# Optimization experiments

Measured on AMD Instinct MI355X. Metric: run time of the kernel, lower is better.

The kernel has to match this reference:

```python
import jax, jax.numpy as jnp
import numpy as np

N_NODES = 100000
N_EDGES = 1600000
F_IN, F_HID, F_OUT = 256, 128, 32


def setup_inputs() -> dict:
    key = jax.random.key(0)
    k1, k2, k3, k4 = jax.random.split(key, 4)
    x = jax.random.normal(k1, (N_NODES, F_IN), dtype=jnp.float32)
    edge_index = jax.random.randint(k2, (2, N_EDGES), 0, N_NODES, dtype=jnp.int64)
    W1 = jax.random.normal(k3, (F_IN, F_HID), dtype=jnp.float32) * (1.0 / np.sqrt(F_IN))
    b1 = jnp.zeros((F_HID,), dtype=jnp.float32)
    W2 = jax.random.normal(k4, (F_HID, F_OUT), dtype=jnp.float32) * (1.0 / np.sqrt(F_HID))
    b2 = jnp.zeros((F_OUT,), dtype=jnp.float32)
    return {"x": x, "edge_index": edge_index, "W1": W1, "b1": b1, "W2": W2, "b2": b2}


def _gcn_norm(edge_index, num_nodes):
    # Add self-loops, then symmetric normalization deg^-1/2[src] * deg^-1/2[dst].
    loops = jnp.arange(num_nodes, dtype=edge_index.dtype)
    src = jnp.concatenate([edge_index[0], loops])
    dst = jnp.concatenate([edge_index[1], loops])
    deg = jax.ops.segment_sum(jnp.ones_like(dst, dtype=jnp.float32), dst,
                              num_segments=num_nodes)
    dinv = jnp.where(deg > 0, jax.lax.rsqrt(deg), 0.0)
    norm = dinv[src] * dinv[dst]  # [E + N]
    return src, dst, norm


def _gcn_conv(h, src, dst, norm, num_nodes):
    # h already linearly transformed. Gather sources, scale, scatter-add to dst.
    msgs = h[src] * norm[:, None]
    return jax.ops.segment_sum(msgs, dst, num_segments=num_nodes)


def reference(x, edge_index, W1, b1, W2, b2):
    n = x.shape[0]
    src, dst, norm = _gcn_norm(edge_index, n)
    # Layer 1: linear -> normalized scatter-add -> bias -> relu
    h = _gcn_conv(x @ W1, src, dst, norm, n) + b1
    h = jax.nn.relu(h)
    # F.dropout with training=False (eval mode) is identity.
    # Layer 2
    out = _gcn_conv(h @ W2, src, dst, norm, n) + b2
    return jax.nn.log_softmax(out, axis=1)
```

## Files before the change

### kernel.cpp

```cpp
#include <hip/hip_runtime.h>

#define N_NODES 100000
#define N_EDGES 1600000
#define F_IN 256
#define F_HID 128
#define F_OUT 32
#define NBUCK 391
#define BIN_BLOCKS 512
#define EDGES_PER_BIN 3125

typedef unsigned short ushort_t;
typedef unsigned int uint_t;

using short8  = __attribute__((ext_vector_type(8))) short;
using floatx4 = __attribute__((ext_vector_type(4))) float;

__device__ __forceinline__ ushort_t f2bf(float f) {
    uint_t u = __float_as_uint(f);
    u += 0x7fff + ((u >> 16) & 1);
    return (ushort_t)(u >> 16);
}
__device__ __forceinline__ float bf_lo(uint_t u) { return __uint_as_float(u << 16); }
__device__ __forceinline__ float bf_hi(uint_t u) { return __uint_as_float(u & 0xffff0000u); }

__global__ __launch_bounds__(256) void hist_kernel(const int* __restrict__ ei,
                                                   int* __restrict__ bucket_cnt) {
    __shared__ int h[NBUCK];
    for (int i = threadIdx.x; i < NBUCK; i += 256) h[i] = 0;
    __syncthreads();
    int gid = blockIdx.x * 256 + threadIdx.x;
    for (int e = gid; e < N_EDGES; e += BIN_BLOCKS * 256)
        atomicAdd(&h[ei[N_EDGES + e] >> 8], 1);
    __syncthreads();
    for (int i = threadIdx.x; i < NBUCK; i += 256) {
        int c = h[i];
        if (c) atomicAdd(&bucket_cnt[i], c);
    }
}

__global__ __launch_bounds__(512) void scan_kernel(const int* __restrict__ bucket_cnt,
                                                   int* __restrict__ bucket_base,
                                                   int* __restrict__ bucket_cursor,
                                                   int* __restrict__ offs) {
    __shared__ int s[512];
    int t = threadIdx.x;
    int own = (t < NBUCK) ? bucket_cnt[t] : 0;
    s[t] = own;
    __syncthreads();
    for (int off = 1; off < 512; off <<= 1) {
        int v = (t >= off) ? s[t - off] : 0;
        __syncthreads();
        s[t] += v;
        __syncthreads();
    }
    if (t < NBUCK) {
        int ex = s[t] - own;
        bucket_base[t] = ex;
        bucket_cursor[t] = ex;
    }
    if (t == 0) {
        bucket_base[NBUCK] = N_EDGES;
        offs[N_NODES] = N_EDGES;
    }
}

__global__ __launch_bounds__(256) void bin_kernel(const int* __restrict__ ei,
                                                  int* __restrict__ bucket_cursor,
                                                  int2* __restrict__ binned) {
    __shared__ int h[NBUCK];
    __shared__ int base[NBUCK];
    const int t = threadIdx.x;
    const int beg = blockIdx.x * EDGES_PER_BIN;
    const int end = beg + EDGES_PER_BIN;
    for (int i = t; i < NBUCK; i += 256) h[i] = 0;
    __syncthreads();
    for (int e = beg + t; e < end; e += 256) atomicAdd(&h[ei[N_EDGES + e] >> 8], 1);
    __syncthreads();
    for (int i = t; i < NBUCK; i += 256) {
        int c = h[i];
        base[i] = c ? atomicAdd(&bucket_cursor[i], c) : 0;
        h[i] = 0;
    }
    __syncthreads();
    for (int e = beg + t; e < end; e += 256) {
        int s = ei[e], d = ei[N_EDGES + e];
        int bk = d >> 8;
        int p = base[bk] + atomicAdd(&h[bk], 1);
        binned[p] = make_int2(s, d);
    }
}

__global__ __launch_bounds__(256) void build_kernel(const int2* __restrict__ binned,
                                                    const int* __restrict__ bucket_base,
                                                    int* __restrict__ offs,
                                                    int* __restrict__ csr,
                                                    float* __restrict__ dinv) {
    __shared__ int h[256];
    __shared__ int sc[256];
    __shared__ int cur[256];
    const int b = blockIdx.x, t = threadIdx.x;
    const int beg = bucket_base[b];
    const int end = bucket_base[b + 1];
    h[t] = 0;
    __syncthreads();
    for (int j = beg + t; j < end; j += 256) {
        int2 p = binned[j];
        atomicAdd(&h[p.y & 255], 1);
    }
    __syncthreads();
    int deg = h[t];
    sc[t] = deg;
    __syncthreads();
    for (int off = 1; off < 256; off <<= 1) {
        int v = (t >= off) ? sc[t - off] : 0;
        __syncthreads();
        sc[t] += v;
        __syncthreads();
    }
    int excl = sc[t] - deg;
    cur[t] = excl;
    int node = b * 256 + t;
    if (node < N_NODES) {
        offs[node] = beg + excl;
        dinv[node] = rsqrtf((float)deg + 1.0f);
    }
    __syncthreads();
    for (int j = beg + t; j < end; j += 256) {
        int2 p = binned[j];
        int pos = atomicAdd(&cur[p.y & 255], 1);
        csr[beg + pos] = p.x;
    }
}

__global__ __launch_bounds__(256) void w1t_kernel(const float* __restrict__ W1,
                                                  ushort_t* __restrict__ W1T) {
    int t = blockIdx.x * 256 + threadIdx.x;
#pragma unroll
    for (int j = 0; j < 4; j++) {
        int e = j * 8192 + t;
        int n = e >> 8, k = e & 255;
        W1T[e] = f2bf(W1[k * F_HID + n]);
    }
}

__global__ __launch_bounds__(256) void w2t_kernel(const float* __restrict__ W2,
                                                  ushort_t* __restrict__ W2T) {
    int e = blockIdx.x * 256 + threadIdx.x;
    int n = e >> 7, k = e & 127;
    W2T[e] = f2bf(W2[k * F_OUT + n]);
}

__global__ __launch_bounds__(256) void gemm1_kernel(const float* __restrict__ x,
                                                    const ushort_t* __restrict__ W1T,
                                                    ushort_t* __restrict__ h0bf) {
    __shared__ ushort_t Bst[F_HID][F_IN + 8];
    const int tid = threadIdx.x;
    const int rbase = blockIdx.x * 64;
    const int w = tid >> 6;
    const int lane = tid & 63;
    const int q = lane >> 4;
    const int nloc = lane & 15;

#pragma unroll
    for (int j = 0; j < 16; j++) {
        int f = j * 256 + tid;
        int n = f >> 5, kg = f & 31;
        uint4 v = ((const uint4*)(W1T + n * F_IN))[kg];
        *(uint4*)(&Bst[n][kg * 8]) = v;
    }
    __syncthreads();

    const int rowA = rbase + w * 16 + nloc;
    const bool okA = rowA < N_NODES;
    const float* ap = x + (size_t)rowA * F_IN + q * 8;

    floatx4 acc[8];
#pragma unroll
    for (int t = 0; t < 8; t++) acc[t] = (floatx4){0.f, 0.f, 0.f, 0.f};

#pragma unroll
    for (int k0 = 0; k0 < F_IN; k0 += 32) {
        float4 f0 = make_float4(0.f, 0.f, 0.f, 0.f);
        float4 f1 = make_float4(0.f, 0.f, 0.f, 0.f);
        if (okA) {
            f0 = *(const float4*)(ap + k0);
            f1 = *(const float4*)(ap + k0 + 4);
        }
        short8 a;
        a[0] = (short)f2bf(f0.x); a[1] = (short)f2bf(f0.y);
        a[2] = (short)f2bf(f0.z); a[3] = (short)f2bf(f0.w);
        a[4] = (short)f2bf(f1.x); a[5] = (short)f2bf(f1.y);
        a[6] = (short)f2bf(f1.z); a[7] = (short)f2bf(f1.w);
#pragma unroll
        for (int t = 0; t < 8; t++) {
            short8 b = *(const short8*)(&Bst[t * 16 + nloc][k0 + q * 8]);
            acc[t] = __builtin_amdgcn_mfma_f32_16x16x32_bf16(a, b, acc[t], 0, 0, 0);
        }
    }

#pragma unroll
    for (int reg = 0; reg < 4; reg++) {
        int rowD = rbase + w * 16 + q * 4 + reg;
        if (rowD < N_NODES) {
            ushort_t* op = h0bf + (size_t)rowD * F_HID + nloc;
#pragma unroll
            for (int t = 0; t < 8; t++) op[t * 16] = f2bf(acc[t][reg]);
        }
    }
}

__global__ __launch_bounds__(256) void gather128(const ushort_t* __restrict__ h0bf,
                                                 const int* __restrict__ offs,
                                                 const int* __restrict__ csr,
                                                 const float* __restrict__ dinv,
                                                 ushort_t* __restrict__ aggbf) {
    int node = blockIdx.x * 8 + (threadIdx.x >> 5);
    int l = threadIdx.x & 31;
    float dn = dinv[node];
    uint2 sv = ((const uint2*)(h0bf + (size_t)node * F_HID))[l];
    float s = dn * dn;
    float4 acc;
    acc.x = bf_lo(sv.x) * s; acc.y = bf_hi(sv.x) * s;
    acc.z = bf_lo(sv.y) * s; acc.w = bf_hi(sv.y) * s;

    int beg = offs[node], end = offs[node + 1];
    int j = beg;
    for (; j + 3 < end; j += 4) {
        int s0 = csr[j], s1 = csr[j + 1], s2 = csr[j + 2], s3 = csr[j + 3];
        float n0 = dinv[s0] * dn, n1 = dinv[s1] * dn;
        float n2 = dinv[s2] * dn, n3 = dinv[s3] * dn;
        uint2 v0 = ((const uint2*)(h0bf + (size_t)s0 * F_HID))[l];
        uint2 v1 = ((const uint2*)(h0bf + (size_t)s1 * F_HID))[l];
        uint2 v2 = ((const uint2*)(h0bf + (size_t)s2 * F_HID))[l];
        uint2 v3 = ((const uint2*)(h0bf + (size_t)s3 * F_HID))[l];
        acc.x += bf_lo(v0.x) * n0 + bf_lo(v1.x) * n1 + bf_lo(v2.x) * n2 + bf_lo(v3.x) * n3;
        acc.y += bf_hi(v0.x) * n0 + bf_hi(v1.x) * n1 + bf_hi(v2.x) * n2 + bf_hi(v3.x) * n3;
        acc.z += bf_lo(v0.y) * n0 + bf_lo(v1.y) * n1 + bf_lo(v2.y) * n2 + bf_lo(v3.y) * n3;
        acc.w += bf_hi(v0.y) * n0 + bf_hi(v1.y) * n1 + bf_hi(v2.y) * n2 + bf_hi(v3.y) * n3;
    }
    for (; j < end; j++) {
        int s0 = csr[j];
        float n0 = dinv[s0] * dn;
        uint2 v0 = ((const uint2*)(h0bf + (size_t)s0 * F_HID))[l];
        acc.x += bf_lo(v0.x) * n0; acc.y += bf_hi(v0.x) * n0;
        acc.z += bf_lo(v0.y) * n0; acc.w += bf_hi(v0.y) * n0;
    }
    uint2 p;
    p.x = (uint_t)f2bf(acc.x) | ((uint_t)f2bf(acc.y) << 16);
    p.y = (uint_t)f2bf(acc.z) | ((uint_t)f2bf(acc.w) << 16);
    ((uint2*)(aggbf + (size_t)node * F_HID))[l] = p;
}

__global__ __launch_bounds__(256) void gemm2_kernel(const ushort_t* __restrict__ aggbf,
                                                    const float* __restrict__ b1,
                                                    const ushort_t* __restrict__ W2T,
                                                    ushort_t* __restrict__ h2bf) {
    __shared__ ushort_t Bs[F_OUT][F_HID + 8];
    __shared__ float b1s[F_HID];
    const int tid = threadIdx.x;
    const int rbase = blockIdx.x * 64;
    const int w = tid >> 6;
    const int lane = tid & 63;
    const int q = lane >> 4;
    const int nloc = lane & 15;

    if (tid < F_HID) b1s[tid] = b1[tid];
#pragma unroll
    for (int jj = 0; jj < 2; jj++) {
        int f = jj * 256 + tid;
        int n = f >> 4, kg = f & 15;
        uint4 v = ((const uint4*)(W2T + n * F_HID))[kg];
        *(uint4*)(&Bs[n][kg * 8]) = v;
    }
    __syncthreads();

    const int rowA = rbase + w * 16 + nloc;
    const bool okA = rowA < N_NODES;

    floatx4 acc[2];
    acc[0] = (floatx4){0.f, 0.f, 0.f, 0.f};
    acc[1] = (floatx4){0.f, 0.f, 0.f, 0.f};

#pragma unroll
    for (int k0 = 0; k0 < F_HID; k0 += 32) {
        int kk = k0 + q * 8;
        uint4 av = make_uint4(0, 0, 0, 0);
        if (okA) av = *(const uint4*)(aggbf + (size_t)rowA * F_HID + kk);
        float4 bb0 = *(const float4*)(&b1s[kk]);
        float4 bb1 = *(const float4*)(&b1s[kk + 4]);
        short8 a;
        a[0] = (short)f2bf(fmaxf(bf_lo(av.x) + bb0.x, 0.f));
        a[1] = (short)f2bf(fmaxf(bf_hi(av.x) + bb0.y, 0.f));
        a[2] = (short)f2bf(fmaxf(bf_lo(av.y) + bb0.z, 0.f));
        a[3] = (short)f2bf(fmaxf(bf_hi(av.y) + bb0.w, 0.f));
        a[4] = (short)f2bf(fmaxf(bf_lo(av.z) + bb1.x, 0.f));
        a[5] = (short)f2bf(fmaxf(bf_hi(av.z) + bb1.y, 0.f));
        a[6] = (short)f2bf(fmaxf(bf_lo(av.w) + bb1.z, 0.f));
        a[7] = (short)f2bf(fmaxf(bf_hi(av.w) + bb1.w, 0.f));
#pragma unroll
        for (int t = 0; t < 2; t++) {
            short8 b = *(const short8*)(&Bs[t * 16 + nloc][kk]);
            acc[t] = __builtin_amdgcn_mfma_f32_16x16x32_bf16(a, b, acc[t], 0, 0, 0);
        }
    }
#pragma unroll
    for (int reg = 0; reg < 4; reg++) {
        int rowD = rbase + w * 16 + q * 4 + reg;
        if (rowD < N_NODES) {
            ushort_t* op = h2bf + (size_t)rowD * F_OUT + nloc;
            op[0]  = f2bf(acc[0][reg]);
            op[16] = f2bf(acc[1][reg]);
        }
    }
}

__global__ __launch_bounds__(256) void gather32_lsm(const ushort_t* __restrict__ h2bf,
                                                    const int* __restrict__ offs,
                                                    const int* __restrict__ csr,
                                                    const float* __restrict__ dinv,
                                                    const float* __restrict__ b2,
                                                    float* __restrict__ out) {
    int node = blockIdx.x * 32 + (threadIdx.x >> 3);
    int l = threadIdx.x & 7;
    float dn = dinv[node];
    uint2 sv = ((const uint2*)(h2bf + (size_t)node * F_OUT))[l];
    float s = dn * dn;
    float4 acc;
    acc.x = bf_lo(sv.x) * s; acc.y = bf_hi(sv.x) * s;
    acc.z = bf_lo(sv.y) * s; acc.w = bf_hi(sv.y) * s;

    int beg = offs[node], end = offs[node + 1];
    int j = beg;
    for (; j + 3 < end; j += 4) {
        int s0 = csr[j], s1 = csr[j + 1], s2 = csr[j + 2], s3 = csr[j + 3];
        float n0 = dinv[s0] * dn, n1 = dinv[s1] * dn;
        float n2 = dinv[s2] * dn, n3 = dinv[s3] * dn;
        uint2 v0 = ((const uint2*)(h2bf + (size_t)s0 * F_OUT))[l];
        uint2 v1 = ((const uint2*)(h2bf + (size_t)s1 * F_OUT))[l];
        uint2 v2 = ((const uint2*)(h2bf + (size_t)s2 * F_OUT))[l];
        uint2 v3 = ((const uint2*)(h2bf + (size_t)s3 * F_OUT))[l];
        acc.x += bf_lo(v0.x) * n0 + bf_lo(v1.x) * n1 + bf_lo(v2.x) * n2 + bf_lo(v3.x) * n3;
        acc.y += bf_hi(v0.x) * n0 + bf_hi(v1.x) * n1 + bf_hi(v2.x) * n2 + bf_hi(v3.x) * n3;
        acc.z += bf_lo(v0.y) * n0 + bf_lo(v1.y) * n1 + bf_lo(v2.y) * n2 + bf_lo(v3.y) * n3;
        acc.w += bf_hi(v0.y) * n0 + bf_hi(v1.y) * n1 + bf_hi(v2.y) * n2 + bf_hi(v3.y) * n3;
    }
    for (; j < end; j++) {
        int s0 = csr[j];
        float n0 = dinv[s0] * dn;
        uint2 v0 = ((const uint2*)(h2bf + (size_t)s0 * F_OUT))[l];
        acc.x += bf_lo(v0.x) * n0; acc.y += bf_hi(v0.x) * n0;
        acc.z += bf_lo(v0.y) * n0; acc.w += bf_hi(v0.y) * n0;
    }
    float4 bb = ((const float4*)b2)[l];
    acc.x += bb.x; acc.y += bb.y; acc.z += bb.z; acc.w += bb.w;

    float m = fmaxf(fmaxf(acc.x, acc.y), fmaxf(acc.z, acc.w));
#pragma unroll
    for (int off = 1; off < 8; off <<= 1) m = fmaxf(m, __shfl_xor(m, off, 8));
    float es = __expf(acc.x - m) + __expf(acc.y - m) + __expf(acc.z - m) + __expf(acc.w - m);
#pragma unroll
    for (int off = 1; off < 8; off <<= 1) es += __shfl_xor(es, off, 8);
    float lse = m + __logf(es);
    float4 o = make_float4(acc.x - lse, acc.y - lse, acc.z - lse, acc.w - lse);
    ((float4*)(out + (size_t)node * F_OUT))[l] = o;
}

extern "C" void kernel_launch(void* const* d_in, const int* in_sizes, int n_in,
                              void* d_out, int out_size, void* d_ws, size_t ws_size,
                              hipStream_t stream) {
    const float* x  = (const float*)d_in[0];
    const int*   ei = (const int*)d_in[1];
    const float* W1 = (const float*)d_in[2];
    const float* b1 = (const float*)d_in[3];
    const float* W2 = (const float*)d_in[4];
    const float* b2 = (const float*)d_in[5];
    float* out = (float*)d_out;

    float* ws = (float*)d_ws;
    float*    dinv          = ws;
    int*      offs          = (int*)(ws + 100096);
    int*      bucket_cnt    = (int*)(ws + 200224);
    int*      bucket_base   = (int*)(ws + 200736);
    int*      bucket_cursor = (int*)(ws + 201248);
    int*      csr           = (int*)(ws + 201760);
    ushort_t* W1T           = (ushort_t*)(ws + 1801760);
    ushort_t* W2T           = (ushort_t*)(ws + 1818144);
    ushort_t* h0bf          = (ushort_t*)(ws + 1820192);
    ushort_t* aggbf         = (ushort_t*)(ws + 8220192);
    ushort_t* h2bf          = (ushort_t*)(ws + 14620192);
    int2*     binned        = (int2*)aggbf;

    hipMemsetAsync(bucket_cnt, 0, 512 * sizeof(int), stream);
    hist_kernel<<<BIN_BLOCKS, 256, 0, stream>>>(ei, bucket_cnt);
    scan_kernel<<<1, 512, 0, stream>>>(bucket_cnt, bucket_base, bucket_cursor, offs);
    bin_kernel<<<BIN_BLOCKS, 256, 0, stream>>>(ei, bucket_cursor, binned);
    build_kernel<<<NBUCK, 256, 0, stream>>>(binned, bucket_base, offs, csr, dinv);
    w1t_kernel<<<32, 256, 0, stream>>>(W1, W1T);
    w2t_kernel<<<16, 256, 0, stream>>>(W2, W2T);
    gemm1_kernel<<<(N_NODES + 63) / 64, 256, 0, stream>>>(x, W1T, h0bf);
    gather128<<<N_NODES / 8, 256, 0, stream>>>(h0bf, offs, csr, dinv, aggbf);
    gemm2_kernel<<<(N_NODES + 63) / 64, 256, 0, stream>>>(aggbf, b1, W2T, h2bf);
    gather32_lsm<<<N_NODES / 32, 256, 0, stream>>>(h2bf, offs, csr, dinv, b2, out);
}
```

Baseline: 361.0 us.

## Persist gemm1 blocks, merge weight transposes, unroll gathers by eight

```diff
diff --git a/kernel.cpp b/kernel.cpp
--- a/kernel.cpp
+++ b/kernel.cpp
@@ -8,6 +8,8 @@
 #define NBUCK 391
 #define BIN_BLOCKS 512
 #define EDGES_PER_BIN 3125
+#define G1_BLOCKS 512
+#define G1_TILES 1563
 
 typedef unsigned short ushort_t;
 typedef unsigned int uint_t;
@@ -132,8 +134,10 @@
     }
 }
 
-__global__ __launch_bounds__(256) void w1t_kernel(const float* __restrict__ W1,
-                                                  ushort_t* __restrict__ W1T) {
+__global__ __launch_bounds__(256) void wt_kernel(const float* __restrict__ W1,
+                                                 const float* __restrict__ W2,
+                                                 ushort_t* __restrict__ W1T,
+                                                 ushort_t* __restrict__ W2T) {
     int t = blockIdx.x * 256 + threadIdx.x;
 #pragma unroll
     for (int j = 0; j < 4; j++) {
@@ -141,13 +145,10 @@
         int n = e >> 8, k = e & 255;
         W1T[e] = f2bf(W1[k * F_HID + n]);
     }
-}
-
-__global__ __launch_bounds__(256) void w2t_kernel(const float* __restrict__ W2,
-                                                  ushort_t* __restrict__ W2T) {
-    int e = blockIdx.x * 256 + threadIdx.x;
-    int n = e >> 7, k = e & 127;
-    W2T[e] = f2bf(W2[k * F_OUT + n]);
+    if (t < 4096) {
+        int n = t >> 7, k = t & 127;
+        W2T[t] = f2bf(W2[k * F_OUT + n]);
+    }
 }
 
 __global__ __launch_bounds__(256) void gemm1_kernel(const float* __restrict__ x,
@@ -155,7 +156,6 @@
                                                     ushort_t* __restrict__ h0bf) {
     __shared__ ushort_t Bst[F_HID][F_IN + 8];
     const int tid = threadIdx.x;
-    const int rbase = blockIdx.x * 64;
     const int w = tid >> 6;
     const int lane = tid & 63;
     const int q = lane >> 4;
@@ -170,41 +170,44 @@
     }
     __syncthreads();
 
-    const int rowA = rbase + w * 16 + nloc;
-    const bool okA = rowA < N_NODES;
-    const float* ap = x + (size_t)rowA * F_IN + q * 8;
-
-    floatx4 acc[8];
-#pragma unroll
-    for (int t = 0; t < 8; t++) acc[t] = (floatx4){0.f, 0.f, 0.f, 0.f};
-
-#pragma unroll
-    for (int k0 = 0; k0 < F_IN; k0 += 32) {
-        float4 f0 = make_float4(0.f, 0.f, 0.f, 0.f);
-        float4 f1 = make_float4(0.f, 0.f, 0.f, 0.f);
-        if (okA) {
-            f0 = *(const float4*)(ap + k0);
-            f1 = *(const float4*)(ap + k0 + 4);
-        }
-        short8 a;
-        a[0] = (short)f2bf(f0.x); a[1] = (short)f2bf(f0.y);
-        a[2] = (short)f2bf(f0.z); a[3] = (short)f2bf(f0.w);
-        a[4] = (short)f2bf(f1.x); a[5] = (short)f2bf(f1.y);
-        a[6] = (short)f2bf(f1.z); a[7] = (short)f2bf(f1.w);
-#pragma unroll
-        for (int t = 0; t < 8; t++) {
-            short8 b = *(const short8*)(&Bst[t * 16 + nloc][k0 + q * 8]);
-            acc[t] = __builtin_amdgcn_mfma_f32_16x16x32_bf16(a, b, acc[t], 0, 0, 0);
-        }
-    }
-
-#pragma unroll
-    for (int reg = 0; reg < 4; reg++) {
-        int rowD = rbase + w * 16 + q * 4 + reg;
-        if (rowD < N_NODES) {
-            ushort_t* op = h0bf + (size_t)rowD * F_HID + nloc;
-#pragma unroll
-            for (int t = 0; t < 8; t++) op[t * 16] = f2bf(acc[t][reg]);
+    for (int tile = blockIdx.x; tile < G1_TILES; tile += G1_BLOCKS) {
+        const int rbase = tile * 64;
+        const int rowA = rbase + w * 16 + nloc;
+        const bool okA = rowA < N_NODES;
+        const float* ap = x + (size_t)rowA * F_IN + q * 8;
+
+        floatx4 acc[8];
+#pragma unroll
+        for (int t = 0; t < 8; t++) acc[t] = (floatx4){0.f, 0.f, 0.f, 0.f};
+
+#pragma unroll
+        for (int k0 = 0; k0 < F_IN; k0 += 32) {
+            float4 f0 = make_float4(0.f, 0.f, 0.f, 0.f);
+            float4 f1 = make_float4(0.f, 0.f, 0.f, 0.f);
+            if (okA) {
+                f0 = *(const float4*)(ap + k0);
+                f1 = *(const float4*)(ap + k0 + 4);
+            }
+            short8 a;
+            a[0] = (short)f2bf(f0.x); a[1] = (short)f2bf(f0.y);
+            a[2] = (short)f2bf(f0.z); a[3] = (short)f2bf(f0.w);
+            a[4] = (short)f2bf(f1.x); a[5] = (short)f2bf(f1.y);
+            a[6] = (short)f2bf(f1.z); a[7] = (short)f2bf(f1.w);
+#pragma unroll
+            for (int t = 0; t < 8; t++) {
+                short8 b = *(const short8*)(&Bst[t * 16 + nloc][k0 + q * 8]);
+                acc[t] = __builtin_amdgcn_mfma_f32_16x16x32_bf16(a, b, acc[t], 0, 0, 0);
+            }
+        }
+
+#pragma unroll
+        for (int reg = 0; reg < 4; reg++) {
+            int rowD = rbase + w * 16 + q * 4 + reg;
+            if (rowD < N_NODES) {
+                ushort_t* op = h0bf + (size_t)rowD * F_HID + nloc;
+#pragma unroll
+                for (int t = 0; t < 8; t++) op[t * 16] = f2bf(acc[t][reg]);
+            }
         }
     }
 }
@@ -225,18 +228,23 @@
 
     int beg = offs[node], end = offs[node + 1];
     int j = beg;
-    for (; j + 3 < end; j += 4) {
-        int s0 = csr[j], s1 = csr[j + 1], s2 = csr[j + 2], s3 = csr[j + 3];
-        float n0 = dinv[s0] * dn, n1 = dinv[s1] * dn;
-        float n2 = dinv[s2] * dn, n3 = dinv[s3] * dn;
-        uint2 v0 = ((const uint2*)(h0bf + (size_t)s0 * F_HID))[l];
-        uint2 v1 = ((const uint2*)(h0bf + (size_t)s1 * F_HID))[l];
-        uint2 v2 = ((const uint2*)(h0bf + (size_t)s2 * F_HID))[l];
-        uint2 v3 = ((const uint2*)(h0bf + (size_t)s3 * F_HID))[l];
-        acc.x += bf_lo(v0.x) * n0 + bf_lo(v1.x) * n1 + bf_lo(v2.x) * n2 + bf_lo(v3.x) * n3;
-        acc.y += bf_hi(v0.x) * n0 + bf_hi(v1.x) * n1 + bf_hi(v2.x) * n2 + bf_hi(v3.x) * n3;
-        acc.z += bf_lo(v0.y) * n0 + bf_lo(v1.y) * n1 + bf_lo(v2.y) * n2 + bf_lo(v3.y) * n3;
-        acc.w += bf_hi(v0.y) * n0 + bf_hi(v1.y) * n1 + bf_hi(v2.y) * n2 + bf_hi(v3.y) * n3;
+    for (; j + 7 < end; j += 8) {
+        int si[8];
+        float nn[8];
+        uint2 vv[8];
+#pragma unroll
+        for (int u = 0; u < 8; u++) si[u] = csr[j + u];
+#pragma unroll
+        for (int u = 0; u < 8; u++) vv[u] = ((const uint2*)(h0bf + (size_t)si[u] * F_HID))[l];
+#pragma unroll
+        for (int u = 0; u < 8; u++) nn[u] = dinv[si[u]] * dn;
+#pragma unroll
+        for (int u = 0; u < 8; u++) {
+            acc.x += bf_lo(vv[u].x) * nn[u];
+            acc.y += bf_hi(vv[u].x) * nn[u];
+            acc.z += bf_lo(vv[u].y) * nn[u];
+            acc.w += bf_hi(vv[u].y) * nn[u];
+        }
     }
     for (; j < end; j++) {
         int s0 = csr[j];
@@ -331,18 +339,23 @@
 
     int beg = offs[node], end = offs[node + 1];
     int j = beg;
-    for (; j + 3 < end; j += 4) {
-        int s0 = csr[j], s1 = csr[j + 1], s2 = csr[j + 2], s3 = csr[j + 3];
-        float n0 = dinv[s0] * dn, n1 = dinv[s1] * dn;
-        float n2 = dinv[s2] * dn, n3 = dinv[s3] * dn;
-        uint2 v0 = ((const uint2*)(h2bf + (size_t)s0 * F_OUT))[l];
-        uint2 v1 = ((const uint2*)(h2bf + (size_t)s1 * F_OUT))[l];
-        uint2 v2 = ((const uint2*)(h2bf + (size_t)s2 * F_OUT))[l];
-        uint2 v3 = ((const uint2*)(h2bf + (size_t)s3 * F_OUT))[l];
-        acc.x += bf_lo(v0.x) * n0 + bf_lo(v1.x) * n1 + bf_lo(v2.x) * n2 + bf_lo(v3.x) * n3;
-        acc.y += bf_hi(v0.x) * n0 + bf_hi(v1.x) * n1 + bf_hi(v2.x) * n2 + bf_hi(v3.x) * n3;
-        acc.z += bf_lo(v0.y) * n0 + bf_lo(v1.y) * n1 + bf_lo(v2.y) * n2 + bf_lo(v3.y) * n3;
-        acc.w += bf_hi(v0.y) * n0 + bf_hi(v1.y) * n1 + bf_hi(v2.y) * n2 + bf_hi(v3.y) * n3;
+    for (; j + 7 < end; j += 8) {
+        int si[8];
+        float nn[8];
+        uint2 vv[8];
+#pragma unroll
+        for (int u = 0; u < 8; u++) si[u] = csr[j + u];
+#pragma unroll
+        for (int u = 0; u < 8; u++) vv[u] = ((const uint2*)(h2bf + (size_t)si[u] * F_OUT))[l];
+#pragma unroll
+        for (int u = 0; u < 8; u++) nn[u] = dinv[si[u]] * dn;
+#pragma unroll
+        for (int u = 0; u < 8; u++) {
+            acc.x += bf_lo(vv[u].x) * nn[u];
+            acc.y += bf_hi(vv[u].x) * nn[u];
+            acc.z += bf_lo(vv[u].y) * nn[u];
+            acc.w += bf_hi(vv[u].y) * nn[u];
+        }
     }
     for (; j < end; j++) {
         int s0 = csr[j];
@@ -395,9 +408,8 @@
     scan_kernel<<<1, 512, 0, stream>>>(bucket_cnt, bucket_base, bucket_cursor, offs);
     bin_kernel<<<BIN_BLOCKS, 256, 0, stream>>>(ei, bucket_cursor, binned);
     build_kernel<<<NBUCK, 256, 0, stream>>>(binned, bucket_base, offs, csr, dinv);
-    w1t_kernel<<<32, 256, 0, stream>>>(W1, W1T);
-    w2t_kernel<<<16, 256, 0, stream>>>(W2, W2T);
-    gemm1_kernel<<<(N_NODES + 63) / 64, 256, 0, stream>>>(x, W1T, h0bf);
+    wt_kernel<<<32, 256, 0, stream>>>(W1, W2, W1T, W2T);
+    gemm1_kernel<<<G1_BLOCKS, 256, 0, stream>>>(x, W1T, h0bf);
     gather128<<<N_NODES / 8, 256, 0, stream>>>(h0bf, offs, csr, dinv, aggbf);
     gemm2_kernel<<<(N_NODES + 63) / 64, 256, 0, stream>>>(aggbf, b1, W2T, h2bf);
     gather32_lsm<<<N_NODES / 32, 256, 0, stream>>>(h2bf, offs, csr, dinv, b2, out);
```

Result: slower. 378.6 us (+4.9%).
